# Kernel tuning notes

Measured on AMD Instinct MI355X. Metric: run time of the kernel, lower is better.

The kernel has to match this reference:

```python
import jax, jax.numpy as jnp
import numpy as np

NUM_TOKENS = 4096
LATENT_DIM = 256
BETA = 0.25
TEMPERATURE = 1.0  # temp_init buffer value
EPS_TEMP = 1e-6


def setup_inputs() -> dict:
    key = jax.random.key(0)
    k1, k2 = jax.random.split(key)
    latent = jax.random.normal(k1, (4, 2048, LATENT_DIM), dtype=jnp.float32)
    cb = jax.random.normal(k2, (NUM_TOKENS, LATENT_DIM), dtype=jnp.float32)
    # module normalizes codebook rows at init
    codebook = cb / jnp.linalg.norm(cb, axis=-1, keepdims=True)
    return {"latent": latent, "codebook": codebook}


def _l2norm(x):
    return x / jnp.clip(jnp.linalg.norm(x, axis=-1, keepdims=True), 1e-12)


def reference(latent, codebook):
    B, S, D = latent.shape
    flat = latent.reshape(-1, D)                       # [N, D]
    # cosine similarity via normalized matmul
    ln = _l2norm(flat)
    cn = _l2norm(codebook)
    cosine_sim = jnp.einsum('nd,kd->nk', ln, cn)       # [N, K]
    distances = 2.0 - 2.0 * cosine_sim
    scaled = distances / jnp.maximum(TEMPERATURE, EPS_TEMP)
    soft_assign = jax.nn.softmax(-scaled, axis=-1)     # [N, K]
    indices = jnp.argmax(soft_assign, axis=-1)         # [N]
    hard_assign = jax.nn.one_hot(indices, NUM_TOKENS, dtype=jnp.float32)
    # straight-through soft->hard assignment
    assign = hard_assign + soft_assign - jax.lax.stop_gradient(soft_assign)

    selected_cosine_sim = jnp.take_along_axis(cosine_sim, indices[:, None], axis=1).mean()

    # codebook pairwise euclidean diagnostics (off-diagonal mean / min)
    sq = jnp.sum(codebook * codebook, axis=-1)         # [K]
    d2 = sq[:, None] + sq[None, :] - 2.0 * (codebook @ codebook.T)
    cdist = jnp.sqrt(jnp.clip(d2, 0.0))                # [K, K]
    K = NUM_TOKENS
    off_sum = jnp.sum(cdist) - jnp.sum(jnp.diagonal(cdist))
    avg_euclidean = off_sum / (K * (K - 1))
    eye = jnp.eye(K, dtype=bool)
    min_euclidean = jnp.min(jnp.where(eye, jnp.inf, cdist))

    quantized = (assign @ codebook).reshape(B, S, D)
    commitment_loss = BETA * jnp.mean((jax.lax.stop_gradient(latent) - quantized) ** 2)
    codebook_loss = jnp.mean((latent - jax.lax.stop_gradient(quantized)) ** 2)
    quantized = latent + jax.lax.stop_gradient(quantized - latent)

    avg_probs = jnp.mean(hard_assign, axis=0)
    perplexity = jnp.exp(-jnp.sum(avg_probs * jnp.log(avg_probs + 1e-10)))

    return (quantized, indices, commitment_loss, codebook_loss, perplexity,
            selected_cosine_sim, avg_euclidean, min_euclidean)
```

## Files before the change

### kernel.cpp

```cpp
#include <hip/hip_runtime.h>
#include <hip/hip_bf16.h>
#include <math.h>

#define NTOK 8192
#define DIM 256
#define KCB 4096
#define NCB (KCB / 128)
#define NKEY 4
#define NKROW (NCB * NKEY)
#define DELTA 0.08f
#define GTIE 2e-6
#define MAXC 16
#define NSCOB2 ((NTOK / 256) * (KCB / 256))
#define NTRI2 ((KCB / 256) * (KCB / 256 + 1) / 2)
#define NPAIRB NTRI2

typedef unsigned long long ull;
typedef unsigned short ushort;
typedef __attribute__((ext_vector_type(8))) short shortx8;
typedef __attribute__((ext_vector_type(4))) float floatx4;
typedef const __attribute__((address_space(1))) void* gas_cp;
typedef __attribute__((address_space(3))) void* las_p;

__device__ __forceinline__ unsigned f2ord(float f) {
    unsigned u = __float_as_uint(f);
    return (u & 0x80000000u) ? ~u : (u | 0x80000000u);
}
__device__ __forceinline__ float ord2f(unsigned u) {
    unsigned b = (u & 0x80000000u) ? (u & 0x7FFFFFFFu) : ~u;
    return __uint_as_float(b);
}
__device__ __forceinline__ ushort f2bf(float f) {
    unsigned u = __float_as_uint(f);
    unsigned r = u + 0x7FFFu + ((u >> 16) & 1u);
    return (ushort)(r >> 16);
}

union TileSmem {
    struct { ushort a[256][64]; ushort b[256][64]; } t[2];
    unsigned keys[256][68];
    struct { float rs[512]; float rm[512]; } red;
};

__device__ __forceinline__ void stage_tile8(const ushort* __restrict__ gA,
                                            const ushort* __restrict__ gB,
                                            ushort (*la)[64], ushort (*lb)[64],
                                            int wave, int lane, int kk) {
    int p = lane & 7;
    int rsub = lane >> 3;
    int kc = p ^ rsub;
    const ushort* sa = gA + (size_t)(wave * 32 + rsub) * DIM + kk + kc * 8;
    const ushort* sb = gB + (size_t)(wave * 32 + rsub) * DIM + kk + kc * 8;
#pragma unroll
    for (int c = 0; c < 4; ++c) {
        __builtin_amdgcn_global_load_lds((gas_cp)(sa + (size_t)(c * 8) * DIM),
                                         (las_p)&la[wave * 32 + c * 8][0], 16, 0, 0);
        __builtin_amdgcn_global_load_lds((gas_cp)(sb + (size_t)(c * 8) * DIM),
                                         (las_p)&lb[wave * 32 + c * 8][0], 16, 0, 0);
    }
}
__device__ __forceinline__ shortx8 frag_read(const ushort (*lds)[64], int row,
                                             int lc) {
    return *(const shortx8*)&lds[row][(lc ^ (row & 7)) * 8];
}

__global__ __launch_bounds__(256) void prep(const float* __restrict__ lat,
                                            const float* __restrict__ cb,
                                            float* __restrict__ nrml,
                                            float* __restrict__ nrmc,
                                            ushort* __restrict__ latbf,
                                            ushort* __restrict__ cnbf,
                                            ushort* __restrict__ cbbf,
                                            float* __restrict__ sq,
                                            unsigned* __restrict__ counts) {
    int bid = blockIdx.x, t = threadIdx.x;
    int wid = t >> 6, lane = t & 63;
    int h = (lane >> 3) & 1, j = lane & 7;
    if (bid < NTOK / 4) {
        int n = bid * 4 + wid;
        if (bid < 16) counts[bid * 256 + t] = 0u;
        const float* row = lat + (size_t)n * DIM;
        int d0 = lane * 4;
        float4 xv = *(const float4*)(row + d0);
        ushort4 bv;
        bv.x = f2bf(xv.x); bv.y = f2bf(xv.y); bv.z = f2bf(xv.z); bv.w = f2bf(xv.w);
        *(ushort4*)(latbf + (size_t)n * DIM + d0) = bv;
        const float* p = row + h * 128;
        float r = __fmul_rn(p[j], p[j]);
#pragma unroll
        for (int i = 8; i < 128; i += 8)
            r = __fadd_rn(r, __fmul_rn(p[i + j], p[i + j]));
        float v[16];
#pragma unroll
        for (int l = 0; l < 16; ++l) v[l] = __shfl(r, l, 64);
        float h0 = __fadd_rn(__fadd_rn(__fadd_rn(v[0], v[1]), __fadd_rn(v[2], v[3])),
                             __fadd_rn(__fadd_rn(v[4], v[5]), __fadd_rn(v[6], v[7])));
        float h1 = __fadd_rn(__fadd_rn(__fadd_rn(v[8], v[9]), __fadd_rn(v[10], v[11])),
                             __fadd_rn(__fadd_rn(v[12], v[13]), __fadd_rn(v[14], v[15])));
        float nr = fmaxf(sqrtf(__fadd_rn(h0, h1)), 1e-12f);
        if (lane == 0) nrml[n] = nr;
    } else {
        int n = (bid - NTOK / 4) * 4 + wid;
        const float* row = cb + (size_t)n * DIM;
        int d0 = lane * 4;
        float4 xv = *(const float4*)(row + d0);
        const float* p = row + h * 128;
        float r = __fmul_rn(p[j], p[j]);
        double ds = 0.0;
#pragma unroll
        for (int i = 8; i < 128; i += 8)
            r = __fadd_rn(r, __fmul_rn(p[i + j], p[i + j]));
#pragma unroll
        for (int i = 0; i < 128; i += 8) { double vv = (double)p[i + j]; ds += vv * vv; }
        float v[16];
#pragma unroll
        for (int l = 0; l < 16; ++l) v[l] = __shfl(r, l, 64);
        float h0 = __fadd_rn(__fadd_rn(__fadd_rn(v[0], v[1]), __fadd_rn(v[2], v[3])),
                             __fadd_rn(__fadd_rn(v[4], v[5]), __fadd_rn(v[6], v[7])));
        float h1 = __fadd_rn(__fadd_rn(__fadd_rn(v[8], v[9]), __fadd_rn(v[10], v[11])),
                             __fadd_rn(__fadd_rn(v[12], v[13]), __fadd_rn(v[14], v[15])));
        float nr = fmaxf(sqrtf(__fadd_rn(h0, h1)), 1e-12f);
#pragma unroll
        for (int off = 1; off < 16; off <<= 1) ds += __shfl_xor(ds, off, 16);
        if (lane == 0) { nrmc[n] = nr; sq[n] = (float)ds; }
        ushort4 cn, cbv;
        cn.x = f2bf(xv.x / nr); cn.y = f2bf(xv.y / nr);
        cn.z = f2bf(xv.z / nr); cn.w = f2bf(xv.w / nr);
        cbv.x = f2bf(xv.x); cbv.y = f2bf(xv.y); cbv.z = f2bf(xv.z); cbv.w = f2bf(xv.w);
        *(ushort4*)(cnbf + (size_t)n * DIM + d0) = cn;
        *(ushort4*)(cbbf + (size_t)n * DIM + d0) = cbv;
    }
}

__global__ __launch_bounds__(512, 2) void gemms(const ushort* __restrict__ latbf,
                                                const ushort* __restrict__ cnbf,
                                                const ushort* __restrict__ cbbf,
                                                const float* __restrict__ sq,
                                                unsigned* __restrict__ keysw,
                                                float* __restrict__ psumw,
                                                unsigned* __restrict__ pminw) {
    __shared__ TileSmem sm;
    int tid = threadIdx.x;
    int wave = tid >> 6, lane = tid & 63;
    int quad = lane >> 4, l15 = lane & 15;
    int wr = wave >> 1, wc = wave & 1;
    bool isScore = blockIdx.x < NSCOB2;
    int rowBase, colBase, tri = 0, cbk = 0;
    const ushort *gA, *gB;
    if (isScore) {
        cbk = blockIdx.x & 15;
        int rbk = blockIdx.x >> 4;
        rowBase = rbk * 256; colBase = cbk * 256;
        gA = latbf + (size_t)rowBase * DIM;
        gB = cnbf + (size_t)colBase * DIM;
    } else {
        tri = blockIdx.x - NSCOB2;
        int a = (int)((sqrtf(8.f * tri + 1.f) - 1.f) * 0.5f);
        while ((a + 1) * (a + 2) / 2 <= tri) ++a;
        while (a * (a + 1) / 2 > tri) --a;
        int b = tri - a * (a + 1) / 2;
        rowBase = b * 256; colBase = a * 256;
        gA = cbbf + (size_t)rowBase * DIM;
        gB = cbbf + (size_t)colBase * DIM;
    }
    floatx4 acc[4][8];
#pragma unroll
    for (int m = 0; m < 4; ++m)
#pragma unroll
        for (int n = 0; n < 8; ++n) acc[m][n] = (floatx4){0.f, 0.f, 0.f, 0.f};

    stage_tile8(gA, gB, sm.t[0].a, sm.t[0].b, wave, lane, 0);
    stage_tile8(gA, gB, sm.t[1].a, sm.t[1].b, wave, lane, 64);
#pragma unroll
    for (int t = 0; t < 4; ++t) {
        int cur = t & 1;
        if (t < 3)
            asm volatile("s_waitcnt vmcnt(8)" ::: "memory");
        else
            asm volatile("s_waitcnt vmcnt(0)" ::: "memory");
        __builtin_amdgcn_s_barrier();
#pragma unroll
        for (int s = 0; s < 2; ++s) {
            shortx8 af[4], bfv[8];
#pragma unroll
            for (int mt = 0; mt < 4; ++mt)
                af[mt] = frag_read(sm.t[cur].a, wr * 64 + mt * 16 + l15, s * 4 + quad);
#pragma unroll
            for (int nt = 0; nt < 8; ++nt)
                bfv[nt] = frag_read(sm.t[cur].b, wc * 128 + nt * 16 + l15, s * 4 + quad);
            __builtin_amdgcn_s_setprio(1);
#pragma unroll
            for (int mt = 0; mt < 4; ++mt)
#pragma unroll
                for (int nt = 0; nt < 8; ++nt)
                    acc[mt][nt] = __builtin_amdgcn_mfma_f32_16x16x32_bf16(
                        af[mt], bfv[nt], acc[mt][nt], 0, 0, 0);
            __builtin_amdgcn_s_setprio(0);
        }
        __builtin_amdgcn_s_barrier();
        if (t < 2)
            stage_tile8(gA, gB, sm.t[cur].a, sm.t[cur].b, wave, lane, (t + 2) * 64);
    }
    __syncthreads();
    if (isScore) {
        unsigned colp2[8];
#pragma unroll
        for (int nt = 0; nt < 8; ++nt)
            colp2[nt] = 0x80000000u | (4095u - (unsigned)(colBase + wc * 128 + nt * 16 + l15));
#pragma unroll
        for (int mt = 0; mt < 4; ++mt)
#pragma unroll
            for (int reg = 0; reg < 4; ++reg) {
                unsigned b1 = 0u, b2 = 0u;
#pragma unroll
                for (int nt = 0; nt < 8; ++nt) {
                    unsigned key = (__float_as_uint(fmaxf(acc[mt][nt][reg], 0.f)) & 0x7FFFF000u)
                                   | colp2[nt];
                    unsigned lo = min(key, b1);
                    b1 = max(key, b1);
                    b2 = max(lo, b2);
                }
                int row = wr * 64 + mt * 16 + quad * 4 + reg;
                uint2 kv; kv.x = b1; kv.y = b2;
                *(uint2*)&sm.keys[row][(wc * 16 + l15) * 2] = kv;
            }
        __syncthreads();
        {
            int prow = tid >> 1, hh = tid & 1;
            unsigned a0 = 0, a1 = 0, a2 = 0, a3 = 0;
#pragma unroll
            for (int j2 = 0; j2 < 8; ++j2) {
                uint4 v4 = *(const uint4*)&sm.keys[prow][hh * 32 + j2 * 4];
                unsigned vs[4] = {v4.x, v4.y, v4.z, v4.w};
#pragma unroll
                for (int q = 0; q < 4; ++q) {
                    unsigned v = vs[q];
                    unsigned n0 = min(v, a0); a0 = max(v, a0);
                    unsigned n1 = min(n0, a1); a1 = max(n0, a1);
                    unsigned n2 = min(n1, a2); a2 = max(n1, a2);
                    a3 = max(n2, a3);
                }
            }
            size_t base = (size_t)(rowBase + prow) * NKROW + (size_t)(cbk * 2 + hh) * NKEY;
            uint4 o; o.x = a0; o.y = a1; o.z = a2; o.w = a3;
            *(uint4*)&keysw[base] = o;
        }
    } else {
        float lsum = 0.f, lmin = INFINITY;
#pragma unroll
        for (int mt = 0; mt < 4; ++mt)
#pragma unroll
            for (int reg = 0; reg < 4; ++reg) {
                int i = rowBase + wr * 64 + mt * 16 + quad * 4 + reg;
                float sqi = sq[i];
#pragma unroll
                for (int nt = 0; nt < 8; ++nt) {
                    int j2 = colBase + wc * 128 + nt * 16 + l15;
                    float d2 = sqi + sq[j2] - 2.0f * acc[mt][nt][reg];
                    float d = sqrtf(fmaxf(d2, 0.0f));
                    bool use = i < j2;
                    lsum += use ? d : 0.f;
                    lmin = fminf(lmin, use ? d : INFINITY);
                }
            }
        sm.red.rs[tid] = lsum; sm.red.rm[tid] = lmin; __syncthreads();
        for (int s = 256; s > 0; s >>= 1) {
            if (tid < s) {
                sm.red.rs[tid] += sm.red.rs[tid + s];
                sm.red.rm[tid] = fminf(sm.red.rm[tid], sm.red.rm[tid + s]);
            }
            __syncthreads();
        }
        if (tid == 0) { psumw[tri] = sm.red.rs[0]; pminw[tri] = f2ord(sm.red.rm[0]); }
    }
}

__global__ __launch_bounds__(256) void argmax_resolve(const float* __restrict__ lat,
                                                      const float* __restrict__ cb,
                                                      const float* __restrict__ nrml,
                                                      const float* __restrict__ nrmc,
                                                      const unsigned* __restrict__ keysw,
                                                      float* __restrict__ outidx,
                                                      float* __restrict__ outq,
                                                      unsigned* __restrict__ counts,
                                                      float* __restrict__ selw,
                                                      float* __restrict__ msew) {
    __shared__ int scand[4][MAXC];
    __shared__ double sc64[4][MAXC];
    int wid = threadIdx.x >> 6, lane = threadIdx.x & 63;
    int n = blockIdx.x * 4 + wid;
    const unsigned* kr = keysw + (size_t)n * NKROW;
    uint2 kv = *(const uint2*)(kr + lane * 2);
    unsigned m = max(kv.x, kv.y);
#pragma unroll
    for (int off = 1; off < 64; off <<= 1) {
        unsigned o = __shfl_xor(m, off, 64);
        m = max(m, o);
    }
    float v1 = ord2f(m & 0xFFFFF000u);
    float thresh = v1 - DELTA;
    bool p0 = ord2f(kv.x & 0xFFFFF000u) >= thresh;
    bool p1 = ord2f(kv.y & 0xFFFFF000u) >= thresh;
    ull b0 = __ballot(p0), b1 = __ballot(p1);
    int below0 = __builtin_amdgcn_mbcnt_hi((unsigned)(b0 >> 32),
                 __builtin_amdgcn_mbcnt_lo((unsigned)b0, 0));
    int below1 = __builtin_amdgcn_mbcnt_hi((unsigned)(b1 >> 32),
                 __builtin_amdgcn_mbcnt_lo((unsigned)b1, 0));
    int base1 = __popcll(b0);
    int nc = base1 + __popcll(b1);
    if (p0 && below0 < MAXC)
        scand[wid][below0] = 4095 - (int)(kv.x & 0xFFFu);
    if (p1 && base1 + below1 < MAXC)
        scand[wid][base1 + below1] = 4095 - (int)(kv.y & 0xFFFu);
    nc = nc < MAXC ? nc : MAXC;
    __threadfence_block();
    float nx = nrml[n];
    int d0 = lane * 4;
    float4 xv = *(const float4*)(lat + (size_t)n * DIM + d0);
    int idx; float selcos;
    if (nc <= 1) {
        idx = 4095 - (int)(m & 0xFFFu);
        selcos = v1 / nx;
    } else {
        float la0 = xv.x / nx, la1 = xv.y / nx, la2 = xv.z / nx, la3 = xv.w / nx;
        for (int c = 0; c < nc; ++c) {
            int k = scand[wid][c];
            float nk = nrmc[k];
            float4 cv = *(const float4*)(cb + (size_t)k * DIM + d0);
            double part = (double)(cv.x / nk) * la0 + (double)(cv.y / nk) * la1 +
                          (double)(cv.z / nk) * la2 + (double)(cv.w / nk) * la3;
#pragma unroll
            for (int off = 1; off < 64; off <<= 1) part += __shfl_xor(part, off, 64);
            if (lane == 0) sc64[wid][c] = part;
        }
        __threadfence_block();
        double best64 = -1e300;
        for (int c = 0; c < nc; ++c) best64 = fmax(best64, sc64[wid][c]);
        int nrisk = 0;
        for (int c = 0; c < nc; ++c) if (sc64[wid][c] >= best64 - GTIE) ++nrisk;
        if (nrisk == 1) {
            idx = 0x7FFFFFFF; selcos = 0.f;
            for (int c = 0; c < nc; ++c)
                if (sc64[wid][c] >= best64 - GTIE) { idx = scand[wid][c]; selcos = (float)sc64[wid][c]; }
        } else {
            ull keyf = 0ull, keym = 0ull;
            if (lane < nc && sc64[wid][lane] >= best64 - GTIE) {
                int k = scand[wid][lane];
                const float* cr = cb + (size_t)k * DIM;
                const float* x = lat + (size_t)n * DIM;
                float nk = nrmc[k];
                float af = 0.f, am = 0.f;
                for (int d = 0; d < DIM; ++d) {
                    float la = x[d] / nx;
                    float cv = cr[d] / nk;
                    af = fmaf(la, cv, af);
                    am = __fadd_rn(am, __fmul_rn(la, cv));
                }
                float df = __fsub_rn(2.0f, __fmul_rn(2.0f, af));
                float dm = __fsub_rn(2.0f, __fmul_rn(2.0f, am));
                keyf = ((ull)(0xFFFFFFFFu - f2ord(df)) << 32) | (ull)(0xFFFFFFFFu - (unsigned)k);
                keym = ((ull)(0xFFFFFFFFu - f2ord(dm)) << 32) | (ull)(0xFFFFFFFFu - (unsigned)k);
            }
#pragma unroll
            for (int off = 1; off < 64; off <<= 1) {
                ull of = __shfl_xor(keyf, off, 64);
                ull om = __shfl_xor(keym, off, 64);
                keyf = of > keyf ? of : keyf;
                keym = om > keym ? om : keym;
            }
            int colf = (int)(0xFFFFFFFFu - (unsigned)(keyf & 0xFFFFFFFFull));
            int colm = (int)(0xFFFFFFFFu - (unsigned)(keym & 0xFFFFFFFFull));
            idx = colf < colm ? colf : colm;
            selcos = 0.f;
            for (int c = 0; c < nc; ++c)
                if (scand[wid][c] == idx) selcos = (float)sc64[wid][c];
        }
    }
    float4 qv = *(const float4*)(cb + (size_t)idx * DIM + d0);
    *(float4*)(outq + (size_t)n * DIM + d0) = qv;
    float dx = xv.x - qv.x, dy = xv.y - qv.y, dz = xv.z - qv.z, dw = xv.w - qv.w;
    float msep = fmaf(dx, dx, fmaf(dy, dy, fmaf(dz, dz, dw * dw)));
#pragma unroll
    for (int off = 1; off < 64; off <<= 1) msep += __shfl_xor(msep, off, 64);
    if (lane == 0) {
        outidx[n] = (float)idx;
        atomicAdd(&counts[idx], 1u);
        selw[n] = selcos;
        msew[n] = msep;
    }
}

__global__ void finalize(const unsigned* __restrict__ counts,
                         const float* __restrict__ selw,
                         const float* __restrict__ msew,
                         const float* __restrict__ psumw,
                         const unsigned* __restrict__ pminw,
                         float* __restrict__ outs) {
    int t = threadIdx.x;
    __shared__ float red[256];
    float h = 0.f;
    for (int k = t; k < KCB; k += 256) {
        float p = (float)counts[k] * (1.0f / (float)NTOK);
        h += p * logf(p + 1e-10f);
    }
    red[t] = h; __syncthreads();
    for (int s = 128; s > 0; s >>= 1) { if (t < s) red[t] += red[t + s]; __syncthreads(); }
    float entNeg = red[0];
    __syncthreads();
    float ssel = 0.f;
    for (int k = t; k < NTOK; k += 256) ssel += selw[k];
    red[t] = ssel; __syncthreads();
    for (int s = 128; s > 0; s >>= 1) { if (t < s) red[t] += red[t + s]; __syncthreads(); }
    float selSum = red[0];
    __syncthreads();
    float sm = 0.f;
    for (int k = t; k < NTOK; k += 256) sm += msew[k];
    red[t] = sm; __syncthreads();
    for (int s = 128; s > 0; s >>= 1) { if (t < s) red[t] += red[t + s]; __syncthreads(); }
    float mseSum = red[0];
    __syncthreads();
    float ps = 0.f;
    for (int k = t; k < NPAIRB; k += 256) ps += psumw[k];
    red[t] = ps; __syncthreads();
    for (int s = 128; s > 0; s >>= 1) { if (t < s) red[t] += red[t + s]; __syncthreads(); }
    float pairSum = red[0];
    __syncthreads();
    unsigned pm = 0xFFFFFFFFu;
    for (int k = t; k < NPAIRB; k += 256) pm = min(pm, pminw[k]);
    ((unsigned*)red)[t] = pm; __syncthreads();
    for (int s = 128; s > 0; s >>= 1) {
        if (t < s) ((unsigned*)red)[t] = min(((unsigned*)red)[t], ((unsigned*)red)[t + s]);
        __syncthreads();
    }
    unsigned pairMin = ((unsigned*)red)[0];
    if (t == 0) {
        float mse = mseSum / (float)(NTOK * DIM);
        outs[0] = 0.25f * mse;
        outs[1] = mse;
        outs[2] = expf(-entNeg);
        outs[3] = selSum / (float)NTOK;
        outs[4] = pairSum * 2.0f / ((float)KCB * (float)(KCB - 1));
        outs[5] = ord2f(pairMin);
    }
}

extern "C" void kernel_launch(void* const* d_in, const int* in_sizes, int n_in,
                              void* d_out, int out_size, void* d_ws, size_t ws_size,
                              hipStream_t stream) {
    const float* latent = (const float*)d_in[0];
    const float* codebook = (const float*)d_in[1];
    float* out = (float*)d_out;
    float* outq = out;
    float* outidx = out + (size_t)NTOK * DIM;
    float* outs = outidx + NTOK;

    unsigned* keysw = (unsigned*)d_ws;
    ushort* latbf = (ushort*)(keysw + (size_t)NKROW * NTOK);
    ushort* cnbf = latbf + (size_t)NTOK * DIM;
    ushort* cbbf = cnbf + (size_t)KCB * DIM;
    float* nrml = (float*)(cbbf + (size_t)KCB * DIM);
    float* nrmc = nrml + NTOK;
    float* sq = nrmc + KCB;
    unsigned* counts = (unsigned*)(sq + KCB);
    float* selw = (float*)(counts + KCB);
    float* msew = selw + NTOK;
    float* psumw = msew + NTOK;
    unsigned* pminw = (unsigned*)(psumw + 528);

    hipLaunchKernelGGL(prep, dim3(NTOK / 4 + KCB / 4), dim3(256), 0, stream,
                       latent, codebook, nrml, nrmc, latbf, cnbf, cbbf, sq, counts);
    hipLaunchKernelGGL(gemms, dim3(NSCOB2 + NTRI2), dim3(512), 0, stream,
                       latbf, cnbf, cbbf, sq, keysw, psumw, pminw);
    hipLaunchKernelGGL(argmax_resolve, dim3(NTOK / 4), dim3(256), 0, stream,
                       latent, codebook, nrml, nrmc, keysw, outidx, outq, counts, selw, msew);
    hipLaunchKernelGGL(finalize, dim3(1), dim3(256), 0, stream, counts, selw, msew, psumw, pminw, outs);
}
```

Baseline: 165.1 us.

## Replace LDS-staged 256x256 GEMM tiles with direct-global-load 128x128 tiles

The fused score/pairwise GEMM kernel drops its LDS double-buffered async staging and reads MFMA fragments directly from global memory. Tiles shrink from 256x256 to 128x128 and the block size from 512 to 256 threads, with occupancy raised to 3 blocks per SIMD. This removes barriers and LDS traffic and makes the grid finer-grained. The cost is less on-chip reuse, more redundant global/L2 traffic, and poorly coalesced 16-byte row loads.

```diff
diff --git a/kernel.cpp b/kernel.cpp
--- a/kernel.cpp
+++ b/kernel.cpp
@@ -11,16 +11,13 @@
 #define DELTA 0.08f
 #define GTIE 2e-6
 #define MAXC 16
-#define NSCOB2 ((NTOK / 256) * (KCB / 256))
-#define NTRI2 ((KCB / 256) * (KCB / 256 + 1) / 2)
-#define NPAIRB NTRI2
+#define NSCOB ((NTOK / 128) * NCB)
+#define NPAIRB (NCB * (NCB + 1) / 2)
 
 typedef unsigned long long ull;
 typedef unsigned short ushort;
 typedef __attribute__((ext_vector_type(8))) short shortx8;
 typedef __attribute__((ext_vector_type(4))) float floatx4;
-typedef const __attribute__((address_space(1))) void* gas_cp;
-typedef __attribute__((address_space(3))) void* las_p;
 
 __device__ __forceinline__ unsigned f2ord(float f) {
     unsigned u = __float_as_uint(f);
@@ -34,34 +31,6 @@
     unsigned u = __float_as_uint(f);
     unsigned r = u + 0x7FFFu + ((u >> 16) & 1u);
     return (ushort)(r >> 16);
-}
-
-union TileSmem {
-    struct { ushort a[256][64]; ushort b[256][64]; } t[2];
-    unsigned keys[256][68];
-    struct { float rs[512]; float rm[512]; } red;
-};
-
-__device__ __forceinline__ void stage_tile8(const ushort* __restrict__ gA,
-                                            const ushort* __restrict__ gB,
-                                            ushort (*la)[64], ushort (*lb)[64],
-                                            int wave, int lane, int kk) {
-    int p = lane & 7;
-    int rsub = lane >> 3;
-    int kc = p ^ rsub;
-    const ushort* sa = gA + (size_t)(wave * 32 + rsub) * DIM + kk + kc * 8;
-    const ushort* sb = gB + (size_t)(wave * 32 + rsub) * DIM + kk + kc * 8;
-#pragma unroll
-    for (int c = 0; c < 4; ++c) {
-        __builtin_amdgcn_global_load_lds((gas_cp)(sa + (size_t)(c * 8) * DIM),
-                                         (las_p)&la[wave * 32 + c * 8][0], 16, 0, 0);
-        __builtin_amdgcn_global_load_lds((gas_cp)(sb + (size_t)(c * 8) * DIM),
-                                         (las_p)&lb[wave * 32 + c * 8][0], 16, 0, 0);
-    }
-}
-__device__ __forceinline__ shortx8 frag_read(const ushort (*lds)[64], int row,
-                                             int lc) {
-    return *(const shortx8*)&lds[row][(lc ^ (row & 7)) * 8];
 }
 
 __global__ __launch_bounds__(256) void prep(const float* __restrict__ lat,
@@ -132,83 +101,69 @@
     }
 }
 
-__global__ __launch_bounds__(512, 2) void gemms(const ushort* __restrict__ latbf,
+__global__ __launch_bounds__(256, 3) void gemms(const ushort* __restrict__ latbf,
                                                 const ushort* __restrict__ cnbf,
                                                 const ushort* __restrict__ cbbf,
                                                 const float* __restrict__ sq,
                                                 unsigned* __restrict__ keysw,
                                                 float* __restrict__ psumw,
                                                 unsigned* __restrict__ pminw) {
-    __shared__ TileSmem sm;
+    __shared__ union {
+        unsigned keys[128][68];
+        struct { float rs[256]; float rm[256]; } red;
+    } sm;
     int tid = threadIdx.x;
-    int wave = tid >> 6, lane = tid & 63;
+    int w = tid >> 6, lane = tid & 63;
     int quad = lane >> 4, l15 = lane & 15;
-    int wr = wave >> 1, wc = wave & 1;
-    bool isScore = blockIdx.x < NSCOB2;
+    bool isScore = blockIdx.x < NSCOB;
     int rowBase, colBase, tri = 0, cbk = 0;
     const ushort *gA, *gB;
     if (isScore) {
-        cbk = blockIdx.x & 15;
-        int rbk = blockIdx.x >> 4;
-        rowBase = rbk * 256; colBase = cbk * 256;
-        gA = latbf + (size_t)rowBase * DIM;
-        gB = cnbf + (size_t)colBase * DIM;
+        cbk = blockIdx.x & (NCB - 1);
+        rowBase = (blockIdx.x >> 5) * 128;
+        colBase = cbk * 128;
+        gA = latbf; gB = cnbf;
     } else {
-        tri = blockIdx.x - NSCOB2;
+        tri = blockIdx.x - NSCOB;
         int a = (int)((sqrtf(8.f * tri + 1.f) - 1.f) * 0.5f);
         while ((a + 1) * (a + 2) / 2 <= tri) ++a;
         while (a * (a + 1) / 2 > tri) --a;
         int b = tri - a * (a + 1) / 2;
-        rowBase = b * 256; colBase = a * 256;
-        gA = cbbf + (size_t)rowBase * DIM;
-        gB = cbbf + (size_t)colBase * DIM;
-    }
-    floatx4 acc[4][8];
-#pragma unroll
-    for (int m = 0; m < 4; ++m)
+        rowBase = b * 128; colBase = a * 128;
+        gA = cbbf; gB = cbbf;
+    }
+    const ushort* pa0 = gA + (size_t)(rowBase + w * 32 + l15) * DIM;
+    const ushort* pa1 = pa0 + (size_t)16 * DIM;
+    const ushort* pb[8];
+#pragma unroll
+    for (int nt = 0; nt < 8; ++nt)
+        pb[nt] = gB + (size_t)(colBase + nt * 16 + l15) * DIM;
+
+    floatx4 acc[2][8];
+#pragma unroll
+    for (int m = 0; m < 2; ++m)
 #pragma unroll
         for (int n = 0; n < 8; ++n) acc[m][n] = (floatx4){0.f, 0.f, 0.f, 0.f};
 
-    stage_tile8(gA, gB, sm.t[0].a, sm.t[0].b, wave, lane, 0);
-    stage_tile8(gA, gB, sm.t[1].a, sm.t[1].b, wave, lane, 64);
-#pragma unroll
-    for (int t = 0; t < 4; ++t) {
-        int cur = t & 1;
-        if (t < 3)
-            asm volatile("s_waitcnt vmcnt(8)" ::: "memory");
-        else
-            asm volatile("s_waitcnt vmcnt(0)" ::: "memory");
-        __builtin_amdgcn_s_barrier();
-#pragma unroll
-        for (int s = 0; s < 2; ++s) {
-            shortx8 af[4], bfv[8];
-#pragma unroll
-            for (int mt = 0; mt < 4; ++mt)
-                af[mt] = frag_read(sm.t[cur].a, wr * 64 + mt * 16 + l15, s * 4 + quad);
-#pragma unroll
-            for (int nt = 0; nt < 8; ++nt)
-                bfv[nt] = frag_read(sm.t[cur].b, wc * 128 + nt * 16 + l15, s * 4 + quad);
-            __builtin_amdgcn_s_setprio(1);
-#pragma unroll
-            for (int mt = 0; mt < 4; ++mt)
-#pragma unroll
-                for (int nt = 0; nt < 8; ++nt)
-                    acc[mt][nt] = __builtin_amdgcn_mfma_f32_16x16x32_bf16(
-                        af[mt], bfv[nt], acc[mt][nt], 0, 0, 0);
-            __builtin_amdgcn_s_setprio(0);
+#pragma unroll 2
+    for (int kk = 0; kk < DIM; kk += 32) {
+        int off = kk + quad * 8;
+        shortx8 a0 = *(const shortx8*)(pa0 + off);
+        shortx8 a1 = *(const shortx8*)(pa1 + off);
+#pragma unroll
+        for (int nt = 0; nt < 8; ++nt) {
+            shortx8 bv = *(const shortx8*)(pb[nt] + off);
+            acc[0][nt] = __builtin_amdgcn_mfma_f32_16x16x32_bf16(a0, bv, acc[0][nt], 0, 0, 0);
+            acc[1][nt] = __builtin_amdgcn_mfma_f32_16x16x32_bf16(a1, bv, acc[1][nt], 0, 0, 0);
         }
-        __builtin_amdgcn_s_barrier();
-        if (t < 2)
-            stage_tile8(gA, gB, sm.t[cur].a, sm.t[cur].b, wave, lane, (t + 2) * 64);
-    }
-    __syncthreads();
+    }
     if (isScore) {
         unsigned colp2[8];
 #pragma unroll
         for (int nt = 0; nt < 8; ++nt)
-            colp2[nt] = 0x80000000u | (4095u - (unsigned)(colBase + wc * 128 + nt * 16 + l15));
-#pragma unroll
-        for (int mt = 0; mt < 4; ++mt)
+            colp2[nt] = 0x80000000u | (4095u - (unsigned)(colBase + nt * 16 + l15));
+#pragma unroll
+        for (int mt = 0; mt < 2; ++mt)
 #pragma unroll
             for (int reg = 0; reg < 4; ++reg) {
                 unsigned b1 = 0u, b2 = 0u;
@@ -220,17 +175,17 @@
                     b1 = max(key, b1);
                     b2 = max(lo, b2);
                 }
-                int row = wr * 64 + mt * 16 + quad * 4 + reg;
+                int row = w * 32 + mt * 16 + quad * 4 + reg;
                 uint2 kv; kv.x = b1; kv.y = b2;
-                *(uint2*)&sm.keys[row][(wc * 16 + l15) * 2] = kv;
+                *(uint2*)&sm.keys[row][l15 * 2] = kv;
             }
         __syncthreads();
-        {
-            int prow = tid >> 1, hh = tid & 1;
+        if (tid < 128) {
+            int row = tid;
             unsigned a0 = 0, a1 = 0, a2 = 0, a3 = 0;
 #pragma unroll
             for (int j2 = 0; j2 < 8; ++j2) {
-                uint4 v4 = *(const uint4*)&sm.keys[prow][hh * 32 + j2 * 4];
+                uint4 v4 = *(const uint4*)&sm.keys[row][j2 * 4];
                 unsigned vs[4] = {v4.x, v4.y, v4.z, v4.w};
 #pragma unroll
                 for (int q = 0; q < 4; ++q) {
@@ -241,21 +196,21 @@
                     a3 = max(n2, a3);
                 }
             }
-            size_t base = (size_t)(rowBase + prow) * NKROW + (size_t)(cbk * 2 + hh) * NKEY;
+            size_t base = (size_t)(rowBase + row) * NKROW + (size_t)cbk * NKEY;
             uint4 o; o.x = a0; o.y = a1; o.z = a2; o.w = a3;
             *(uint4*)&keysw[base] = o;
         }
     } else {
         float lsum = 0.f, lmin = INFINITY;
 #pragma unroll
-        for (int mt = 0; mt < 4; ++mt)
+        for (int mt = 0; mt < 2; ++mt)
 #pragma unroll
             for (int reg = 0; reg < 4; ++reg) {
-                int i = rowBase + wr * 64 + mt * 16 + quad * 4 + reg;
+                int i = rowBase + w * 32 + mt * 16 + quad * 4 + reg;
                 float sqi = sq[i];
 #pragma unroll
                 for (int nt = 0; nt < 8; ++nt) {
-                    int j2 = colBase + wc * 128 + nt * 16 + l15;
+                    int j2 = colBase + nt * 16 + l15;
                     float d2 = sqi + sq[j2] - 2.0f * acc[mt][nt][reg];
                     float d = sqrtf(fmaxf(d2, 0.0f));
                     bool use = i < j2;
@@ -264,7 +219,7 @@
                 }
             }
         sm.red.rs[tid] = lsum; sm.red.rm[tid] = lmin; __syncthreads();
-        for (int s = 256; s > 0; s >>= 1) {
+        for (int s = 128; s > 0; s >>= 1) {
             if (tid < s) {
                 sm.red.rs[tid] += sm.red.rs[tid + s];
                 sm.red.rm[tid] = fminf(sm.red.rm[tid], sm.red.rm[tid + s]);
@@ -465,11 +420,11 @@
     float* selw = (float*)(counts + KCB);
     float* msew = selw + NTOK;
     float* psumw = msew + NTOK;
-    unsigned* pminw = (unsigned*)(psumw + 528);
+    unsigned* pminw = (unsigned*)(psumw + NPAIRB);
 
     hipLaunchKernelGGL(prep, dim3(NTOK / 4 + KCB / 4), dim3(256), 0, stream,
                        latent, codebook, nrml, nrmc, latbf, cnbf, cbbf, sq, counts);
-    hipLaunchKernelGGL(gemms, dim3(NSCOB2 + NTRI2), dim3(512), 0, stream,
+    hipLaunchKernelGGL(gemms, dim3(NSCOB + NPAIRB), dim3(256), 0, stream,
                        latbf, cnbf, cbbf, sq, keysw, psumw, pminw);
     hipLaunchKernelGGL(argmax_resolve, dim3(NTOK / 4), dim3(256), 0, stream,
                        latent, codebook, nrml, nrmc, keysw, outidx, outq, counts, selw, msew);
```

After: 232.8 us. +41.0%, slower.
